# Optimization experiments

Hardware: AMD Instinct MI355X
Metric: run time of the kernel (lower is better)

Reference implementation:

```python
import jax, jax.numpy as jnp
import numpy as np

RATE = 5          # negative_sample_rate
A = 1.0           # _a
BP = 1.0          # _b
REP = 1.0         # repulsion_strength
EPS = 1e-4        # clamp in compute_cross_entropy
BATCH = 65536; C = 100; E = 2048; GN = 16; GP = 5; NIDX = 50000


def setup_inputs() -> dict:
    key = jax.random.key(0)
    ks = jax.random.split(key, 12)
    return {
        'edge_to_idx': jax.random.randint(ks[0], (BATCH,), 0, NIDX),
        'edge_from_idx': jax.random.randint(ks[1], (BATCH,), 0, NIDX),
        'embedding_to': jax.random.normal(ks[2], (BATCH, 2), jnp.float32),
        'embedding_from': jax.random.normal(ks[3], (BATCH, 2), jnp.float32),
        'probs': jax.random.uniform(ks[4], (BATCH,), jnp.float32),
        'pred_edge_to': jax.random.normal(ks[5], (BATCH, C), jnp.float32),
        'pred_edge_from': jax.random.normal(ks[6], (BATCH, C), jnp.float32),
        'perm': jax.random.permutation(ks[7], BATCH * RATE),            # torch.randperm
        'error_conf': jnp.sort(jax.random.randint(ks[8], (E,), 0, NIDX)),
        'neg_grid': jax.random.normal(ks[9], (E, GN, 2), jnp.float32),
        'pos_grid': jax.random.normal(ks[10], (E, GP, 2), jnp.float32),
        'distance_list': jax.random.uniform(ks[11], (E,), jnp.float32),
    }


def _q(d):
    # convert_distance_to_probability: 1 / (1 + a * d^(2b))
    return 1.0 / (1.0 + A * d ** (2.0 * BP))


def _ce_attract(p, q):
    return -p * jnp.log(jnp.clip(q, EPS, 1.0))


def _ce_repulse(p, q):
    return -(1.0 - p) * REP * jnp.log(jnp.clip(1.0 - q, EPS, 1.0))


def _match(idx, error_conf):
    # first position in (sorted) error_conf equal to idx, plus hit mask
    pos = jnp.clip(jnp.searchsorted(error_conf, idx), 0, error_conf.shape[0] - 1)
    return pos, (error_conf[pos] == idx)


def reference(edge_to_idx, edge_from_idx, embedding_to, embedding_from, probs,
              pred_edge_to, pred_edge_from, perm, error_conf, neg_grid,
              pos_grid, distance_list):
    f32 = jnp.float32
    # ---- negative sampling (repeat_interleave + randperm) ----
    emb_neg_to = jnp.repeat(embedding_to, RATE, axis=0)         # [B*R,2]
    pred_neg_to = jnp.repeat(pred_edge_to, RATE, axis=0)        # [B*R,C]
    emb_neg_from = jnp.repeat(embedding_from, RATE, axis=0)[perm]
    pred_neg_from = jnp.repeat(pred_edge_from, RATE, axis=0)[perm]
    # filter_neg: keep where NOT (same argmax AND same max-softmax confidence)
    conf_from = jnp.max(jax.nn.softmax(pred_neg_from, axis=1), axis=1)
    conf_to = jnp.max(jax.nn.softmax(pred_neg_to, axis=1), axis=1)
    same = (jnp.argmax(pred_neg_from, axis=1) == jnp.argmax(pred_neg_to, axis=1)) & (conf_from == conf_to)
    m_neg = (~same).astype(f32)                                 # [B*R]
    neg_dist = jnp.linalg.norm(emb_neg_to - emb_neg_from, axis=1)
    neg_cnt = jnp.sum(m_neg)
    neg_mean = jnp.sum(neg_dist * m_neg) / jnp.maximum(neg_cnt, 1.0)
    # ---- positive distances ----
    pos_dist = jnp.linalg.norm(embedding_to - embedding_from, axis=1)  # [B]
    pos_mean = jnp.mean(pos_dist)
    # ---- confidence-grid pairs (vectorized isin/nonzero loops) ----
    g_to, hit_to = _match(edge_to_idx, error_conf)
    g_from, hit_from = _match(edge_from_idx, error_conf)
    m_to = hit_to.astype(f32)
    m_from = hit_from.astype(f32)
    d_cneg_to = jnp.linalg.norm(embedding_to[:, None, :] - neg_grid[g_to], axis=-1)     # [B,GN]
    d_cneg_from = jnp.linalg.norm(embedding_from[:, None, :] - neg_grid[g_from], axis=-1)
    d_cpos_to = jnp.linalg.norm(embedding_from[:, None, :] - pos_grid[g_to], axis=-1)   # [B,GP]
    d_cpos_from = jnp.linalg.norm(embedding_from[:, None, :] - pos_grid[g_from], axis=-1)
    w_pos_to = m_to * (distance_list[g_to] < 0.5).astype(f32)
    w_pos_from = m_from * (distance_list[g_from] < 1.0).astype(f32)
    # ---- UMAP cross entropy over the concatenated (pos, conf_pos, neg, conf_neg) ----
    ce_pos = _ce_attract(probs, _q(pos_dist)) + _ce_repulse(probs, _q(pos_dist))
    sum_ce = jnp.sum(ce_pos)
    sum_ce += jnp.sum(w_pos_to[:, None] * _ce_attract(1.0, _q(d_cpos_to)))
    sum_ce += jnp.sum(w_pos_from[:, None] * _ce_attract(1.0, _q(d_cpos_from)))
    sum_ce += jnp.sum(m_neg * _ce_repulse(0.0, _q(neg_dist)))
    sum_ce += jnp.sum(m_to[:, None] * _ce_repulse(0.0, _q(d_cneg_to)))
    sum_ce += jnp.sum(m_from[:, None] * _ce_repulse(0.0, _q(d_cneg_from)))
    total_cnt = (pos_dist.shape[0] + GP * (jnp.sum(w_pos_to) + jnp.sum(w_pos_from))
                 + neg_cnt + GN * (jnp.sum(m_to) + jnp.sum(m_from)))
    umap_l = sum_ce / jnp.maximum(total_cnt, 1.0)
    umap_l = jnp.where(jnp.isnan(umap_l), 0.0, umap_l)
    # ---- margin loss ----
    is_pred_same = (jnp.argmax(pred_edge_to, axis=1) == jnp.argmax(pred_edge_from, axis=1)).astype(f32)
    batch_margin = pos_mean + (neg_mean - pos_mean) * (1.0 - probs)
    margin = (1.0 - is_pred_same) * batch_margin
    margin_loss = jnp.mean(jax.nn.relu(margin - pos_dist))
    margin_loss = jnp.where(jnp.isnan(margin_loss), 0.0, margin_loss)
    return (umap_l, margin_loss, umap_l + margin_loss)


if __name__ == '__main__':
    out = reference(**setup_inputs())
    print([float(o) for o in out])
```

## Files before the change

### kernel.cpp

```cpp
#include <hip/hip_runtime.h>
#include <math.h>

#define B_SZ   65536
#define RATE   5
#define NNEG   (B_SZ * RATE)
#define NC     100
#define NE     2048
#define GN     16
#define GP     5
#define EPSC   1e-4f

#define NBN    1280
#define NBP    256
#define NBT    256

__device__ __forceinline__ float wave_sumf(float v) {
    #pragma unroll
    for (int off = 32; off > 0; off >>= 1) v += __shfl_down(v, off, 64);
    return v;
}
__device__ __forceinline__ float clip01(float x) {
    return fminf(fmaxf(x, EPSC), 1.0f);
}

__global__ __launch_bounds__(256, 2) void k_rowstats(
    const float* __restrict__ pred_to, const float* __restrict__ pred_from,
    float2* __restrict__ pk_to, float2* __restrict__ pk_from,
    unsigned int* __restrict__ counter)
{
    if (blockIdx.x == 0 && threadIdx.x == 0) *counter = 0u;
    int gt  = blockIdx.x * 256 + threadIdx.x;
    int wid = gt >> 4;
    int col = gt & 15;
    const float* row = (wid < B_SZ) ? pred_to + (size_t)wid * NC
                                    : pred_from + (size_t)(wid - B_SZ) * NC;
    float4 a = ((const float4*)row)[col];
    float4 b;
    bool hasb = (col < 9);
    if (hasb) b = ((const float4*)row)[16 + col];
    else      b = make_float4(-INFINITY, -INFINITY, -INFINITY, -INFINITY);

    float m = fmaxf(fmaxf(a.x, a.y), fmaxf(a.z, a.w));
    m = fmaxf(m, fmaxf(fmaxf(b.x, b.y), fmaxf(b.z, b.w)));
    #pragma unroll
    for (int mk = 1; mk < 16; mk <<= 1) m = fmaxf(m, __shfl_xor(m, mk, 16));

    int bi = NC;
    int i0 = 4 * col, i1 = 64 + 4 * col;
    if (a.x == m) bi = min(bi, i0 + 0);
    if (a.y == m) bi = min(bi, i0 + 1);
    if (a.z == m) bi = min(bi, i0 + 2);
    if (a.w == m) bi = min(bi, i0 + 3);
    if (b.x == m) bi = min(bi, i1 + 0);
    if (b.y == m) bi = min(bi, i1 + 1);
    if (b.z == m) bi = min(bi, i1 + 2);
    if (b.w == m) bi = min(bi, i1 + 3);
    #pragma unroll
    for (int mk = 1; mk < 16; mk <<= 1) bi = min(bi, __shfl_xor(bi, mk, 16));

    float s = expf(a.x - m) + expf(a.y - m) + expf(a.z - m) + expf(a.w - m)
            + expf(b.x - m) + expf(b.y - m) + expf(b.z - m) + expf(b.w - m);
    #pragma unroll
    for (int mk = 1; mk < 16; mk <<= 1) s += __shfl_xor(s, mk, 16);

    if (col == 0) {
        float2 pk = make_float2(1.0f / s, __uint_as_float((unsigned)bi));
        if (wid < B_SZ) pk_to[wid] = pk; else pk_from[wid - B_SZ] = pk;
    }
}

__global__ __launch_bounds__(256) void k_negpos(
    const int* __restrict__ perm,
    const float2* __restrict__ emb_to, const float2* __restrict__ emb_from,
    const float2* __restrict__ pk_to, const float2* __restrict__ pk_from,
    const int* __restrict__ idx_to, const int* __restrict__ idx_from,
    const float* __restrict__ probs,
    const int* __restrict__ error_conf,
    const float2* __restrict__ neg_grid, const float2* __restrict__ pos_grid,
    const float* __restrict__ dist_list,
    float* __restrict__ pneg, float* __restrict__ ppos)
{
    __shared__ float sr[6][4];
    int w = threadIdx.x >> 6, lane = threadIdx.x & 63;
    if (blockIdx.x < NBN) {
        const unsigned long long* pkt = (const unsigned long long*)pk_to;
        const unsigned long long* pkf = (const unsigned long long*)pk_from;
        int i = blockIdx.x * 256 + threadIdx.x;
        float ce = 0.f, cnt = 0.f, ds = 0.f;
        {
            unsigned jt = (unsigned)i / RATE;
            unsigned jf = (unsigned)perm[i] / RATE;
            if (pkt[jt] != pkf[jf]) {
                float2 et = emb_to[jt], ef = emb_from[jf];
                float dx = et.x - ef.x, dy = et.y - ef.y;
                float d2 = dx * dx + dy * dy;
                float om = d2 / (1.0f + d2);
                ce  = -logf(clip01(om));
                cnt = 1.0f;
                ds  = sqrtf(d2);
            }
        }
        ce = wave_sumf(ce); cnt = wave_sumf(cnt); ds = wave_sumf(ds);
        if (lane == 0) { sr[0][w] = ce; sr[1][w] = cnt; sr[2][w] = ds; }
        __syncthreads();
        if (threadIdx.x < 3) {
            int j = threadIdx.x;
            pneg[blockIdx.x * 3 + j] = sr[j][0] + sr[j][1] + sr[j][2] + sr[j][3];
        }
    } else {
        __shared__ int ec[NE];
        int blk = blockIdx.x - NBN;
        for (int t = threadIdx.x; t < NE; t += 256) ec[t] = error_conf[t];
        __syncthreads();

        float v0 = 0.f, v1 = 0.f, v2 = 0.f, v3 = 0.f, v4 = 0.f, v5 = 0.f;
        {
            int i = blk * 256 + threadIdx.x;
            float2 et = emb_to[i], ef = emb_from[i];
            float dx = et.x - ef.x, dy = et.y - ef.y;
            float d2 = dx * dx + dy * dy;
            v1 = sqrtf(d2);
            float p = probs[i];
            float q  = 1.0f / (1.0f + d2);
            float om = d2 / (1.0f + d2);
            v0 = -p * logf(clip01(q)) - (1.0f - p) * logf(clip01(om));

            int vt = idx_to[i];
            int lo = 0, hi = NE;
            while (lo < hi) { int mid = (lo + hi) >> 1; if (ec[mid] < vt) lo = mid + 1; else hi = mid; }
            int gtd = (lo < NE) ? lo : NE - 1;
            bool hit_t = (ec[gtd] == vt);

            int vf = idx_from[i];
            lo = 0; hi = NE;
            while (lo < hi) { int mid = (lo + hi) >> 1; if (ec[mid] < vf) lo = mid + 1; else hi = mid; }
            int gf = (lo < NE) ? lo : NE - 1;
            bool hit_f = (ec[gf] == vf);

            if (hit_t) {
                v4 = 1.0f;
                float sa = 0.f;
                #pragma unroll
                for (int k2 = 0; k2 < GN; ++k2) {
                    float2 g = neg_grid[gtd * GN + k2];
                    float ax = et.x - g.x, ay = et.y - g.y;
                    float dd = ax * ax + ay * ay;
                    sa += -logf(clip01(dd / (1.0f + dd)));
                }
                v0 += sa;
                if (dist_list[gtd] < 0.5f) {
                    v2 = 1.0f;
                    float s2 = 0.f;
                    #pragma unroll
                    for (int k2 = 0; k2 < GP; ++k2) {
                        float2 g = pos_grid[gtd * GP + k2];
                        float ax = ef.x - g.x, ay = ef.y - g.y;
                        float dd = ax * ax + ay * ay;
                        s2 += -logf(clip01(1.0f / (1.0f + dd)));
                    }
                    v0 += s2;
                }
            }
            if (hit_f) {
                v5 = 1.0f;
                float sa = 0.f;
                #pragma unroll
                for (int k2 = 0; k2 < GN; ++k2) {
                    float2 g = neg_grid[gf * GN + k2];
                    float ax = ef.x - g.x, ay = ef.y - g.y;
                    float dd = ax * ax + ay * ay;
                    sa += -logf(clip01(dd / (1.0f + dd)));
                }
                v0 += sa;
                if (dist_list[gf] < 1.0f) {
                    v3 = 1.0f;
                    float s2 = 0.f;
                    #pragma unroll
                    for (int k2 = 0; k2 < GP; ++k2) {
                        float2 g = pos_grid[gf * GP + k2];
                        float ax = ef.x - g.x, ay = ef.y - g.y;
                        float dd = ax * ax + ay * ay;
                        s2 += -logf(clip01(1.0f / (1.0f + dd)));
                    }
                    v0 += s2;
                }
            }
        }
        float vv[6] = {v0, v1, v2, v3, v4, v5};
        #pragma unroll
        for (int j = 0; j < 6; ++j) {
            float r = wave_sumf(vv[j]);
            if (lane == 0) sr[j][w] = r;
        }
        __syncthreads();
        if (threadIdx.x < 6) {
            int j = threadIdx.x;
            ppos[blk * 6 + j] = sr[j][0] + sr[j][1] + sr[j][2] + sr[j][3];
        }
    }
}

__global__ __launch_bounds__(256) void k_tail(
    const float2* __restrict__ emb_to, const float2* __restrict__ emb_from,
    const float* __restrict__ probs,
    const float2* __restrict__ pk_to, const float2* __restrict__ pk_from,
    const float* __restrict__ pneg, const float* __restrict__ ppos,
    float* __restrict__ pmar, unsigned int* __restrict__ counter,
    float* __restrict__ out)
{
    __shared__ float sr[8][4];
    __shared__ float tot[8];
    __shared__ bool islast;
    int w = threadIdx.x >> 6, lane = threadIdx.x & 63;

    float s[8] = {0, 0, 0, 0, 0, 0, 0, 0};
    for (int b = threadIdx.x; b < NBN; b += 256) {
        s[0] += pneg[b * 3 + 0]; s[1] += pneg[b * 3 + 1]; s[2] += pneg[b * 3 + 2];
    }
    for (int b = threadIdx.x; b < NBP; b += 256) {
        s[0] += ppos[b * 6 + 0]; s[3] += ppos[b * 6 + 1]; s[4] += ppos[b * 6 + 2];
        s[5] += ppos[b * 6 + 3]; s[6] += ppos[b * 6 + 4]; s[7] += ppos[b * 6 + 5];
    }
    #pragma unroll
    for (int j = 0; j < 8; ++j) {
        float r = wave_sumf(s[j]);
        if (lane == 0) sr[j][w] = r;
    }
    __syncthreads();
    if (threadIdx.x < 8) {
        int j = threadIdx.x;
        tot[j] = sr[j][0] + sr[j][1] + sr[j][2] + sr[j][3];
    }
    __syncthreads();
    float pos_mean = tot[3] * (1.0f / (float)B_SZ);
    float neg_mean = tot[2] / fmaxf(tot[1], 1.0f);

    int i = blockIdx.x * 256 + threadIdx.x;
    float2 et = emb_to[i], ef = emb_from[i];
    float2 at = pk_to[i], af = pk_from[i];
    float dx = et.x - ef.x, dy = et.y - ef.y;
    float d = sqrtf(dx * dx + dy * dy);
    float p = probs[i];
    float bm = pos_mean + (neg_mean - pos_mean) * (1.0f - p);
    float mg = (at.y == af.y) ? 0.0f : bm;
    float ms = fmaxf(mg - d, 0.0f);
    ms = wave_sumf(ms);
    if (lane == 0) sr[0][w] = ms;
    __syncthreads();

    if (threadIdx.x == 0) {
        pmar[blockIdx.x] = sr[0][0] + sr[0][1] + sr[0][2] + sr[0][3];
        __threadfence();
        unsigned old = atomicAdd(counter, 1u);
        islast = (old == NBT - 1);
    }
    __syncthreads();
    if (islast) {
        __threadfence();
        float v = pmar[threadIdx.x];
        v = wave_sumf(v);
        if (lane == 0) sr[1][w] = v;
        __syncthreads();
        if (threadIdx.x == 0) {
            float msum = sr[1][0] + sr[1][1] + sr[1][2] + sr[1][3];
            float total_cnt = (float)B_SZ + (float)GP * (tot[4] + tot[5])
                            + tot[1] + (float)GN * (tot[6] + tot[7]);
            float umap = tot[0] / fmaxf(total_cnt, 1.0f);
            if (isnan(umap)) umap = 0.0f;
            float ml = msum * (1.0f / (float)B_SZ);
            if (isnan(ml)) ml = 0.0f;
            out[0] = umap;
            out[1] = ml;
            out[2] = umap + ml;
        }
    }
}

extern "C" void kernel_launch(void* const* d_in, const int* in_sizes, int n_in,
                              void* d_out, int out_size, void* d_ws, size_t ws_size,
                              hipStream_t stream)
{
    const int*   edge_to_idx   = (const int*)d_in[0];
    const int*   edge_from_idx = (const int*)d_in[1];
    const float* embedding_to  = (const float*)d_in[2];
    const float* embedding_from= (const float*)d_in[3];
    const float* probs         = (const float*)d_in[4];
    const float* pred_to       = (const float*)d_in[5];
    const float* pred_from     = (const float*)d_in[6];
    const int*   perm          = (const int*)d_in[7];
    const int*   error_conf    = (const int*)d_in[8];
    const float* neg_grid      = (const float*)d_in[9];
    const float* pos_grid      = (const float*)d_in[10];
    const float* dist_list     = (const float*)d_in[11];

    char* ws = (char*)d_ws;
    unsigned int* counter = (unsigned int*)ws;
    float2*       pk_to   = (float2*)(ws + 256);
    float2*       pk_from = pk_to + B_SZ;
    float*        pneg    = (float*)(pk_from + B_SZ);
    float*        ppos    = pneg + NBN * 3;
    float*        pmar    = ppos + NBP * 6;

    k_rowstats<<<(2 * B_SZ * 16) / 256, 256, 0, stream>>>(
        pred_to, pred_from, pk_to, pk_from, counter);

    k_negpos<<<NBN + NBP, 256, 0, stream>>>(
        perm, (const float2*)embedding_to, (const float2*)embedding_from,
        pk_to, pk_from,
        edge_to_idx, edge_from_idx, probs, error_conf,
        (const float2*)neg_grid, (const float2*)pos_grid, dist_list,
        pneg, ppos);

    k_tail<<<NBT, 256, 0, stream>>>(
        (const float2*)embedding_to, (const float2*)embedding_from,
        probs, pk_to, pk_from, pneg, ppos, pmar, counter, (float*)d_out);
}
```

Baseline: 44.37 us.

## Fuse tail reduction into negpos kernel via spin-wait grid barrier and pack embeddings

Removes the third kernel launch by having the 256 positive-edge blocks spin on a global counter until all 1536 blocks have written partials, then compute the margin loss and final output in place. Row stats now pack the embedding alongside the inverse-sum and argmax into a float4, so negative-sample gathers hit one 16-byte record per side instead of separate pk and embedding arrays. The spin barrier depends on all blocks being co-resident or on the negative blocks finishing first, and the pk buffers double in size.

```diff
diff --git a/kernel.cpp b/kernel.cpp
--- a/kernel.cpp
+++ b/kernel.cpp
@@ -12,7 +12,7 @@
 
 #define NBN    1280
 #define NBP    256
-#define NBT    256
+#define NBK2   (NBN + NBP)
 
 __device__ __forceinline__ float wave_sumf(float v) {
     #pragma unroll
@@ -25,10 +25,11 @@
 
 __global__ __launch_bounds__(256, 2) void k_rowstats(
     const float* __restrict__ pred_to, const float* __restrict__ pred_from,
-    float2* __restrict__ pk_to, float2* __restrict__ pk_from,
-    unsigned int* __restrict__ counter)
+    const float2* __restrict__ emb_to, const float2* __restrict__ emb_from,
+    float4* __restrict__ pk4_to, float4* __restrict__ pk4_from,
+    unsigned int* __restrict__ cnt1, unsigned int* __restrict__ cnt2)
 {
-    if (blockIdx.x == 0 && threadIdx.x == 0) *counter = 0u;
+    if (blockIdx.x == 0 && threadIdx.x == 0) { *cnt1 = 0u; *cnt2 = 0u; }
     int gt  = blockIdx.x * 256 + threadIdx.x;
     int wid = gt >> 4;
     int col = gt & 15;
@@ -36,9 +37,8 @@
                                     : pred_from + (size_t)(wid - B_SZ) * NC;
     float4 a = ((const float4*)row)[col];
     float4 b;
-    bool hasb = (col < 9);
-    if (hasb) b = ((const float4*)row)[16 + col];
-    else      b = make_float4(-INFINITY, -INFINITY, -INFINITY, -INFINITY);
+    if (col < 9) b = ((const float4*)row)[16 + col];
+    else         b = make_float4(-INFINITY, -INFINITY, -INFINITY, -INFINITY);
 
     float m = fmaxf(fmaxf(a.x, a.y), fmaxf(a.z, a.w));
     m = fmaxf(m, fmaxf(fmaxf(b.x, b.y), fmaxf(b.z, b.w)));
@@ -64,35 +64,44 @@
     for (int mk = 1; mk < 16; mk <<= 1) s += __shfl_xor(s, mk, 16);
 
     if (col == 0) {
-        float2 pk = make_float2(1.0f / s, __uint_as_float((unsigned)bi));
-        if (wid < B_SZ) pk_to[wid] = pk; else pk_from[wid - B_SZ] = pk;
-    }
-}
-
-__global__ __launch_bounds__(256) void k_negpos(
+        float2 e = (wid < B_SZ) ? emb_to[wid] : emb_from[wid - B_SZ];
+        float4 pk = make_float4(1.0f / s, __uint_as_float((unsigned)bi), e.x, e.y);
+        if (wid < B_SZ) pk4_to[wid] = pk; else pk4_from[wid - B_SZ] = pk;
+    }
+}
+
+__global__ __launch_bounds__(256, 8) void k_fused(
     const int* __restrict__ perm,
+    const float4* __restrict__ pk4_to, const float4* __restrict__ pk4_from,
     const float2* __restrict__ emb_to, const float2* __restrict__ emb_from,
-    const float2* __restrict__ pk_to, const float2* __restrict__ pk_from,
     const int* __restrict__ idx_to, const int* __restrict__ idx_from,
     const float* __restrict__ probs,
     const int* __restrict__ error_conf,
     const float2* __restrict__ neg_grid, const float2* __restrict__ pos_grid,
     const float* __restrict__ dist_list,
-    float* __restrict__ pneg, float* __restrict__ ppos)
+    float* __restrict__ pneg, float* __restrict__ ppos,
+    float* __restrict__ pmar,
+    unsigned int* __restrict__ cnt1, unsigned int* __restrict__ cnt2,
+    float* __restrict__ out)
 {
-    __shared__ float sr[6][4];
+    __shared__ float sr[8][4];
+    __shared__ int ec[NE];
+    __shared__ float tot[8];
+    __shared__ bool islast;
     int w = threadIdx.x >> 6, lane = threadIdx.x & 63;
+
     if (blockIdx.x < NBN) {
-        const unsigned long long* pkt = (const unsigned long long*)pk_to;
-        const unsigned long long* pkf = (const unsigned long long*)pk_from;
         int i = blockIdx.x * 256 + threadIdx.x;
         float ce = 0.f, cnt = 0.f, ds = 0.f;
         {
             unsigned jt = (unsigned)i / RATE;
             unsigned jf = (unsigned)perm[i] / RATE;
-            if (pkt[jt] != pkf[jf]) {
-                float2 et = emb_to[jt], ef = emb_from[jf];
-                float dx = et.x - ef.x, dy = et.y - ef.y;
+            float4 t4 = pk4_to[jt];
+            float4 f4 = pk4_from[jf];
+            bool same = (__float_as_uint(t4.x) == __float_as_uint(f4.x)) &&
+                        (__float_as_uint(t4.y) == __float_as_uint(f4.y));
+            if (!same) {
+                float dx = t4.z - f4.z, dy = t4.w - f4.w;
                 float d2 = dx * dx + dy * dy;
                 float om = d2 / (1.0f + d2);
                 ce  = -logf(clip01(om));
@@ -107,124 +116,130 @@
             int j = threadIdx.x;
             pneg[blockIdx.x * 3 + j] = sr[j][0] + sr[j][1] + sr[j][2] + sr[j][3];
         }
-    } else {
-        __shared__ int ec[NE];
-        int blk = blockIdx.x - NBN;
-        for (int t = threadIdx.x; t < NE; t += 256) ec[t] = error_conf[t];
+        __threadfence();
         __syncthreads();
-
-        float v0 = 0.f, v1 = 0.f, v2 = 0.f, v3 = 0.f, v4 = 0.f, v5 = 0.f;
-        {
-            int i = blk * 256 + threadIdx.x;
-            float2 et = emb_to[i], ef = emb_from[i];
-            float dx = et.x - ef.x, dy = et.y - ef.y;
-            float d2 = dx * dx + dy * dy;
-            v1 = sqrtf(d2);
-            float p = probs[i];
-            float q  = 1.0f / (1.0f + d2);
-            float om = d2 / (1.0f + d2);
-            v0 = -p * logf(clip01(q)) - (1.0f - p) * logf(clip01(om));
-
-            int vt = idx_to[i];
-            int lo = 0, hi = NE;
-            while (lo < hi) { int mid = (lo + hi) >> 1; if (ec[mid] < vt) lo = mid + 1; else hi = mid; }
-            int gtd = (lo < NE) ? lo : NE - 1;
-            bool hit_t = (ec[gtd] == vt);
-
-            int vf = idx_from[i];
-            lo = 0; hi = NE;
-            while (lo < hi) { int mid = (lo + hi) >> 1; if (ec[mid] < vf) lo = mid + 1; else hi = mid; }
-            int gf = (lo < NE) ? lo : NE - 1;
-            bool hit_f = (ec[gf] == vf);
-
-            if (hit_t) {
-                v4 = 1.0f;
-                float sa = 0.f;
+        if (threadIdx.x == 0) atomicAdd(cnt1, 1u);
+        return;
+    }
+
+    int blk = blockIdx.x - NBN;
+    for (int t = threadIdx.x; t < NE; t += 256) ec[t] = error_conf[t];
+    __syncthreads();
+
+    float v0 = 0.f, v1 = 0.f, v2 = 0.f, v3 = 0.f, v4 = 0.f, v5 = 0.f;
+    {
+        int i = blk * 256 + threadIdx.x;
+        float2 et = emb_to[i], ef = emb_from[i];
+        float dx = et.x - ef.x, dy = et.y - ef.y;
+        float d2 = dx * dx + dy * dy;
+        v1 = sqrtf(d2);
+        float p = probs[i];
+        float q  = 1.0f / (1.0f + d2);
+        float om = d2 / (1.0f + d2);
+        v0 = -p * logf(clip01(q)) - (1.0f - p) * logf(clip01(om));
+
+        int vt = idx_to[i];
+        int lo = 0, hi = NE;
+        while (lo < hi) { int mid = (lo + hi) >> 1; if (ec[mid] < vt) lo = mid + 1; else hi = mid; }
+        int gtd = (lo < NE) ? lo : NE - 1;
+        bool hit_t = (ec[gtd] == vt);
+
+        int vf = idx_from[i];
+        lo = 0; hi = NE;
+        while (lo < hi) { int mid = (lo + hi) >> 1; if (ec[mid] < vf) lo = mid + 1; else hi = mid; }
+        int gf = (lo < NE) ? lo : NE - 1;
+        bool hit_f = (ec[gf] == vf);
+
+        if (hit_t) {
+            v4 = 1.0f;
+            float sa = 0.f;
+            #pragma unroll
+            for (int k2 = 0; k2 < GN; ++k2) {
+                float2 g = neg_grid[gtd * GN + k2];
+                float ax = et.x - g.x, ay = et.y - g.y;
+                float dd = ax * ax + ay * ay;
+                sa += -logf(clip01(dd / (1.0f + dd)));
+            }
+            v0 += sa;
+            if (dist_list[gtd] < 0.5f) {
+                v2 = 1.0f;
+                float s2 = 0.f;
                 #pragma unroll
-                for (int k2 = 0; k2 < GN; ++k2) {
-                    float2 g = neg_grid[gtd * GN + k2];
-                    float ax = et.x - g.x, ay = et.y - g.y;
-                    float dd = ax * ax + ay * ay;
-                    sa += -logf(clip01(dd / (1.0f + dd)));
-                }
-                v0 += sa;
-                if (dist_list[gtd] < 0.5f) {
-                    v2 = 1.0f;
-                    float s2 = 0.f;
-                    #pragma unroll
-                    for (int k2 = 0; k2 < GP; ++k2) {
-                        float2 g = pos_grid[gtd * GP + k2];
-                        float ax = ef.x - g.x, ay = ef.y - g.y;
-                        float dd = ax * ax + ay * ay;
-                        s2 += -logf(clip01(1.0f / (1.0f + dd)));
-                    }
-                    v0 += s2;
-                }
-            }
-            if (hit_f) {
-                v5 = 1.0f;
-                float sa = 0.f;
-                #pragma unroll
-                for (int k2 = 0; k2 < GN; ++k2) {
-                    float2 g = neg_grid[gf * GN + k2];
+                for (int k2 = 0; k2 < GP; ++k2) {
+                    float2 g = pos_grid[gtd * GP + k2];
                     float ax = ef.x - g.x, ay = ef.y - g.y;
                     float dd = ax * ax + ay * ay;
-                    sa += -logf(clip01(dd / (1.0f + dd)));
+                    s2 += -logf(clip01(1.0f / (1.0f + dd)));
                 }
-                v0 += sa;
-                if (dist_list[gf] < 1.0f) {
-                    v3 = 1.0f;
-                    float s2 = 0.f;
-                    #pragma unroll
-                    for (int k2 = 0; k2 < GP; ++k2) {
-                        float2 g = pos_grid[gf * GP + k2];
-                        float ax = ef.x - g.x, ay = ef.y - g.y;
-                        float dd = ax * ax + ay * ay;
-                        s2 += -logf(clip01(1.0f / (1.0f + dd)));
-                    }
-                    v0 += s2;
+                v0 += s2;
+            }
+        }
+        if (hit_f) {
+            v5 = 1.0f;
+            float sa = 0.f;
+            #pragma unroll
+            for (int k2 = 0; k2 < GN; ++k2) {
+                float2 g = neg_grid[gf * GN + k2];
+                float ax = ef.x - g.x, ay = ef.y - g.y;
+                float dd = ax * ax + ay * ay;
+                sa += -logf(clip01(dd / (1.0f + dd)));
+            }
+            v0 += sa;
+            if (dist_list[gf] < 1.0f) {
+                v3 = 1.0f;
+                float s2 = 0.f;
+                #pragma unroll
+                for (int k2 = 0; k2 < GP; ++k2) {
+                    float2 g = pos_grid[gf * GP + k2];
+                    float ax = ef.x - g.x, ay = ef.y - g.y;
+                    float dd = ax * ax + ay * ay;
+                    s2 += -logf(clip01(1.0f / (1.0f + dd)));
                 }
-            }
-        }
+                v0 += s2;
+            }
+        }
+    }
+    {
         float vv[6] = {v0, v1, v2, v3, v4, v5};
         #pragma unroll
         for (int j = 0; j < 6; ++j) {
             float r = wave_sumf(vv[j]);
             if (lane == 0) sr[j][w] = r;
         }
-        __syncthreads();
-        if (threadIdx.x < 6) {
-            int j = threadIdx.x;
-            ppos[blk * 6 + j] = sr[j][0] + sr[j][1] + sr[j][2] + sr[j][3];
-        }
-    }
-}
-
-__global__ __launch_bounds__(256) void k_tail(
-    const float2* __restrict__ emb_to, const float2* __restrict__ emb_from,
-    const float* __restrict__ probs,
-    const float2* __restrict__ pk_to, const float2* __restrict__ pk_from,
-    const float* __restrict__ pneg, const float* __restrict__ ppos,
-    float* __restrict__ pmar, unsigned int* __restrict__ counter,
-    float* __restrict__ out)
-{
-    __shared__ float sr[8][4];
-    __shared__ float tot[8];
-    __shared__ bool islast;
-    int w = threadIdx.x >> 6, lane = threadIdx.x & 63;
-
-    float s[8] = {0, 0, 0, 0, 0, 0, 0, 0};
-    for (int b = threadIdx.x; b < NBN; b += 256) {
-        s[0] += pneg[b * 3 + 0]; s[1] += pneg[b * 3 + 1]; s[2] += pneg[b * 3 + 2];
-    }
-    for (int b = threadIdx.x; b < NBP; b += 256) {
-        s[0] += ppos[b * 6 + 0]; s[3] += ppos[b * 6 + 1]; s[4] += ppos[b * 6 + 2];
-        s[5] += ppos[b * 6 + 3]; s[6] += ppos[b * 6 + 4]; s[7] += ppos[b * 6 + 5];
-    }
-    #pragma unroll
-    for (int j = 0; j < 8; ++j) {
-        float r = wave_sumf(s[j]);
-        if (lane == 0) sr[j][w] = r;
+    }
+    __syncthreads();
+    if (threadIdx.x < 6) {
+        int j = threadIdx.x;
+        ppos[blk * 6 + j] = sr[j][0] + sr[j][1] + sr[j][2] + sr[j][3];
+    }
+    __threadfence();
+    __syncthreads();
+    if (threadIdx.x == 0) atomicAdd(cnt1, 1u);
+
+    if (threadIdx.x == 0) {
+        while (__hip_atomic_load(cnt1, __ATOMIC_RELAXED, __HIP_MEMORY_SCOPE_AGENT) < (unsigned)NBK2)
+            __builtin_amdgcn_s_sleep(2);
+    }
+    __syncthreads();
+    __threadfence();
+
+    {
+        float s[8] = {0, 0, 0, 0, 0, 0, 0, 0};
+        for (int b = threadIdx.x; b < NBN; b += 256) {
+            s[0] += pneg[b * 3 + 0]; s[1] += pneg[b * 3 + 1]; s[2] += pneg[b * 3 + 2];
+        }
+        {
+            int b = threadIdx.x & 255;
+            if (b < NBP) {
+                s[0] += ppos[b * 6 + 0]; s[3] += ppos[b * 6 + 1]; s[4] += ppos[b * 6 + 2];
+                s[5] += ppos[b * 6 + 3]; s[6] += ppos[b * 6 + 4]; s[7] += ppos[b * 6 + 5];
+            }
+        }
+        #pragma unroll
+        for (int j = 0; j < 8; ++j) {
+            float r = wave_sumf(s[j]);
+            if (lane == 0) sr[j][w] = r;
+        }
     }
     __syncthreads();
     if (threadIdx.x < 8) {
@@ -235,24 +250,24 @@
     float pos_mean = tot[3] * (1.0f / (float)B_SZ);
     float neg_mean = tot[2] / fmaxf(tot[1], 1.0f);
 
-    int i = blockIdx.x * 256 + threadIdx.x;
-    float2 et = emb_to[i], ef = emb_from[i];
-    float2 at = pk_to[i], af = pk_from[i];
-    float dx = et.x - ef.x, dy = et.y - ef.y;
-    float d = sqrtf(dx * dx + dy * dy);
-    float p = probs[i];
-    float bm = pos_mean + (neg_mean - pos_mean) * (1.0f - p);
-    float mg = (at.y == af.y) ? 0.0f : bm;
-    float ms = fmaxf(mg - d, 0.0f);
-    ms = wave_sumf(ms);
-    if (lane == 0) sr[0][w] = ms;
-    __syncthreads();
-
+    {
+        int i = blk * 256 + threadIdx.x;
+        float4 t4 = pk4_to[i], f4 = pk4_from[i];
+        float dx = t4.z - f4.z, dy = t4.w - f4.w;
+        float d = sqrtf(dx * dx + dy * dy);
+        float p = probs[i];
+        float bm = pos_mean + (neg_mean - pos_mean) * (1.0f - p);
+        float mg = (__float_as_uint(t4.y) == __float_as_uint(f4.y)) ? 0.0f : bm;
+        float ms = fmaxf(mg - d, 0.0f);
+        ms = wave_sumf(ms);
+        if (lane == 0) sr[0][w] = ms;
+    }
+    __syncthreads();
     if (threadIdx.x == 0) {
-        pmar[blockIdx.x] = sr[0][0] + sr[0][1] + sr[0][2] + sr[0][3];
+        pmar[blk] = sr[0][0] + sr[0][1] + sr[0][2] + sr[0][3];
         __threadfence();
-        unsigned old = atomicAdd(counter, 1u);
-        islast = (old == NBT - 1);
+        unsigned old = atomicAdd(cnt2, 1u);
+        islast = (old == NBP - 1);
     }
     __syncthreads();
     if (islast) {
@@ -294,24 +309,23 @@
     const float* dist_list     = (const float*)d_in[11];
 
     char* ws = (char*)d_ws;
-    unsigned int* counter = (unsigned int*)ws;
-    float2*       pk_to   = (float2*)(ws + 256);
-    float2*       pk_from = pk_to + B_SZ;
-    float*        pneg    = (float*)(pk_from + B_SZ);
+    unsigned int* cnt1    = (unsigned int*)ws;
+    unsigned int* cnt2    = (unsigned int*)(ws + 64);
+    float4*       pk4_to  = (float4*)(ws + 256);
+    float4*       pk4_from= pk4_to + B_SZ;
+    float*        pneg    = (float*)(pk4_from + B_SZ);
     float*        ppos    = pneg + NBN * 3;
     float*        pmar    = ppos + NBP * 6;
 
     k_rowstats<<<(2 * B_SZ * 16) / 256, 256, 0, stream>>>(
-        pred_to, pred_from, pk_to, pk_from, counter);
-
-    k_negpos<<<NBN + NBP, 256, 0, stream>>>(
-        perm, (const float2*)embedding_to, (const float2*)embedding_from,
-        pk_to, pk_from,
+        pred_to, pred_from,
+        (const float2*)embedding_to, (const float2*)embedding_from,
+        pk4_to, pk4_from, cnt1, cnt2);
+
+    k_fused<<<NBK2, 256, 0, stream>>>(
+        perm, pk4_to, pk4_from,
+        (const float2*)embedding_to, (const float2*)embedding_from,
         edge_to_idx, edge_from_idx, probs, error_conf,
         (const float2*)neg_grid, (const float2*)pos_grid, dist_list,
-        pneg, ppos);
-
-    k_tail<<<NBT, 256, 0, stream>>>(
-        (const float2*)embedding_to, (const float2*)embedding_from,
-        probs, pk_to, pk_from, pneg, ppos, pmar, counter, (float*)d_out);
-}
+        pneg, ppos, pmar, cnt1, cnt2, (float*)d_out);
+}
```

Result: slower. 158.6 us (+257.4%).
